# Kernel tuning notes

Measured on AMD Instinct MI355X. Metric: run time of the kernel, lower is better.

## Reference

```python
import math
import jax, jax.numpy as jnp
import numpy as np

B, S, D, H = 2, 2048, 1024, 16
DH = D // H
EPS = 1e-5


def setup_inputs() -> dict:
    key = jax.random.key(0)
    ks = jax.random.split(key, 8)
    def lin(k, din, dout):
        return jax.random.normal(k, (din, dout), dtype=jnp.float32) / math.sqrt(din)
    return {
        "x": jax.random.normal(ks[0], (B, S, D), dtype=jnp.float32),
        "attention_mask": jnp.ones((B, S), dtype=jnp.int32),
        "Wq": lin(ks[1], D, D),
        "Wk": lin(ks[2], D, D),
        "Wv": lin(ks[3], D, D),
        "Wo": lin(ks[4], D, D),
        "W1": lin(ks[5], D, 4 * D),
        "W2": lin(ks[6], 2 * D, D),
        "gamma1": jnp.ones((D,), jnp.float32),
        "beta1": jnp.zeros((D,), jnp.float32),
        "gamma2": jnp.ones((D,), jnp.float32),
        "beta2": jnp.zeros((D,), jnp.float32),
    }


def layernorm(x, gamma, beta):
    mu = jnp.mean(x, axis=-1, keepdims=True)
    xc = x - mu
    var = jnp.mean(xc * xc, axis=-1, keepdims=True)
    return gamma * (xc / jnp.sqrt(var + EPS)) + beta


def softmax_last(x):
    x = x - jnp.max(x, axis=-1, keepdims=True)
    e = jnp.exp(x)
    return e / jnp.sum(e, axis=-1, keepdims=True)


def mhsa(x, attention_mask, Wq, Wk, Wv, Wo, causal=True):
    b, s, d = x.shape
    q = (x @ Wq).reshape(b, s, H, DH).transpose(0, 2, 1, 3)  # [b,h,s,dh]
    k = (x @ Wk).reshape(b, s, H, DH).transpose(0, 2, 1, 3)
    v = (x @ Wv).reshape(b, s, H, DH).transpose(0, 2, 1, 3)
    score = jnp.einsum("bhqd,bhkd->bhqk", q, k) / math.sqrt(DH)
    if causal:
        cmask = jnp.tril(jnp.ones((s, s), dtype=bool))
        score = jnp.where(cmask[None, None], score, -jnp.inf)
    key_mask = attention_mask.astype(bool)[:, None, None, :]  # [b,1,1,s]
    score = jnp.where(key_mask, score, -jnp.inf)
    attn = softmax_last(score)
    out = jnp.einsum("bhqk,bhkd->bhqd", attn, v)
    out = out.transpose(0, 2, 1, 3).reshape(b, s, d)
    return out @ Wo


def reference(x, attention_mask, Wq, Wk, Wv, Wo, W1, W2, gamma1, beta1, gamma2, beta2):
    x1 = x + mhsa(layernorm(x, gamma1, beta1), attention_mask, Wq, Wk, Wv, Wo, causal=True)
    h = layernorm(x1, gamma2, beta2) @ W1          # [b,s,4d]
    left, right = h[:, :, : 2 * D], h[:, :, 2 * D :]
    glu = left * jax.nn.sigmoid(right)             # [b,s,2d]
    return x1 + glu @ W2
```

## Files before the change

kernel.cpp:

```cpp
#include <hip/hip_runtime.h>
#include <hip/hip_bf16.h>
#include <math.h>

#define BB 2
#define SS 2048
#define DD 1024
#define HH 16
#define DH 64
#define NTOK (BB * SS)
#define LN_EPS 1e-5f
#define BIGNEG -1e30f

typedef __attribute__((ext_vector_type(8))) short bf16x8;
typedef __attribute__((ext_vector_type(4))) float f32x4;

static __device__ __forceinline__ unsigned short f2bu(float f) {
    __hip_bfloat16 h = __float2bfloat16(f);
    return *(unsigned short*)&h;
}

static __device__ __forceinline__ void async16(const void* g, void* l) {
    __builtin_amdgcn_global_load_lds((const __attribute__((address_space(1))) void*)g,
                                     (__attribute__((address_space(3))) void*)l, 16, 0, 0);
}


__global__ __launch_bounds__(256) void prep_kernel(const float* __restrict__ Wq,
                                                   const float* __restrict__ Wk,
                                                   const float* __restrict__ Wv,
                                                   const float* __restrict__ Wo,
                                                   const float* __restrict__ W1,
                                                   const float* __restrict__ W2,
                                                   __hip_bfloat16* __restrict__ wqkvt,
                                                   __hip_bfloat16* __restrict__ wot,
                                                   __hip_bfloat16* __restrict__ w1t,
                                                   __hip_bfloat16* __restrict__ w2t,
                                                   const float* __restrict__ x,
                                                   const float* __restrict__ gamma,
                                                   const float* __restrict__ beta,
                                                   __hip_bfloat16* __restrict__ lnb) {
    __shared__ float t[32][33];
    __shared__ float red[256];
    const int bid = blockIdx.x;
    const int tid = threadIdx.x;

    if (bid >= 10240) {
        const int row = bid - 10240;
        const float* xp = x + (size_t)row * DD;
        float vals[4];
        float s = 0.f;
#pragma unroll
        for (int i = 0; i < 4; ++i) {
            float v = xp[tid + i * 256];
            vals[i] = v;
            s += v;
        }
        red[tid] = s;
        __syncthreads();
        for (int st = 128; st > 0; st >>= 1) {
            if (tid < st) red[tid] += red[tid + st];
            __syncthreads();
        }
        const float mu = red[0] * (1.0f / DD);
        __syncthreads();
        float sq = 0.f;
#pragma unroll
        for (int i = 0; i < 4; ++i) {
            float d = vals[i] - mu;
            sq += d * d;
        }
        red[tid] = sq;
        __syncthreads();
        for (int st = 128; st > 0; st >>= 1) {
            if (tid < st) red[tid] += red[tid + st];
            __syncthreads();
        }
        const float rinv = rsqrtf(red[0] * (1.0f / DD) + LN_EPS);
        __hip_bfloat16* op = lnb + (size_t)row * DD;
#pragma unroll
        for (int i = 0; i < 4; ++i) {
            int j = tid + i * 256;
            op[j] = __float2bfloat16(gamma[j] * ((vals[i] - mu) * rinv) + beta[j]);
        }
        return;
    }

    const float* W;
    __hip_bfloat16* Wt;
    int K, N, tile;
    if (bid < 4096) {
        const int m = bid >> 10;
        tile = bid & 1023;
        W = (m == 0) ? Wq : (m == 1) ? Wk : (m == 2) ? Wv : Wo;
        Wt = (m < 3) ? (wqkvt + (size_t)m * 1024 * 1024) : wot;
        K = 1024; N = 1024;
    } else if (bid < 8192) {
        tile = bid - 4096; W = W1; Wt = w1t; K = 1024; N = 4096;
    } else {
        tile = bid - 8192; W = W2; Wt = w2t; K = 2048; N = 1024;
    }
    const int nt = N >> 5;
    const int n0 = (tile % nt) * 32, k0 = (tile / nt) * 32;
    const int tx = tid & 31, ty = tid >> 5;
#pragma unroll
    for (int i = 0; i < 4; ++i)
        t[ty + 8 * i][tx] = W[(size_t)(k0 + ty + 8 * i) * N + n0 + tx];
    __syncthreads();
#pragma unroll
    for (int i = 0; i < 4; ++i)
        Wt[(size_t)(n0 + ty + 8 * i) * K + k0 + tx] = __float2bfloat16(t[tx][ty + 8 * i]);
}

__global__ __launch_bounds__(256) void ln_kernel(const float* __restrict__ x,
                                                 const float* __restrict__ gamma,
                                                 const float* __restrict__ beta,
                                                 __hip_bfloat16* __restrict__ out) {
    const int row = blockIdx.x;
    const int tid = threadIdx.x;
    __shared__ float red[256];

    const float* xp = x + (size_t)row * DD;
    float vals[4];
    float s = 0.f;
#pragma unroll
    for (int i = 0; i < 4; ++i) {
        float v = xp[tid + i * 256];
        vals[i] = v;
        s += v;
    }
    red[tid] = s;
    __syncthreads();
    for (int st = 128; st > 0; st >>= 1) {
        if (tid < st) red[tid] += red[tid + st];
        __syncthreads();
    }
    const float mu = red[0] * (1.0f / DD);
    __syncthreads();
    float sq = 0.f;
#pragma unroll
    for (int i = 0; i < 4; ++i) {
        float d = vals[i] - mu;
        sq += d * d;
    }
    red[tid] = sq;
    __syncthreads();
    for (int st = 128; st > 0; st >>= 1) {
        if (tid < st) red[tid] += red[tid + st];
        __syncthreads();
    }
    const float rinv = rsqrtf(red[0] * (1.0f / DD) + LN_EPS);

    __hip_bfloat16* op = out + (size_t)row * DD;
#pragma unroll
    for (int i = 0; i < 4; ++i) {
        int j = tid + i * 256;
        op[j] = __float2bfloat16(gamma[j] * ((vals[i] - mu) * rinv) + beta[j]);
    }
}

__global__ __launch_bounds__(256) void vtrans(const __hip_bfloat16* __restrict__ qkvb_,
                                              __hip_bfloat16* __restrict__ VT_) {
    const unsigned short* src = (const unsigned short*)qkvb_;
    unsigned short* dst = (unsigned short*)VT_;
    __shared__ unsigned short t[64][65];
    const int c0 = (blockIdx.x & 15) << 6;
    const int t0 = (blockIdx.x >> 4) << 6;
    const int tx = threadIdx.x & 63, ty = threadIdx.x >> 6;
#pragma unroll
    for (int i = 0; i < 16; ++i)
        t[ty + 4 * i][tx] = src[(size_t)(t0 + ty + 4 * i) * 3072 + 2048 + c0 + tx];
    __syncthreads();
#pragma unroll
    for (int i = 0; i < 16; ++i)
        dst[(size_t)(c0 + ty + 4 * i) * 4096 + t0 + tx] = t[tx][ty + 4 * i];
}

template <int RES, int EPI>
__global__ __launch_bounds__(256) void mfma_gemm(const __hip_bfloat16* __restrict__ A,
                                                 const __hip_bfloat16* __restrict__ Bt,
                                                 const void* __restrict__ res,
                                                 void* __restrict__ out,
                                                 int M, int N, int K) {
    __shared__ short As[128 * 64];
    __shared__ short Bs[128 * 64];
    const int tid = threadIdx.x;
    const int lane = tid & 63;
    const int wave = tid >> 6;
    const int row0 = blockIdx.y * 128;
    const int col0 = blockIdx.x * 128;
    const int wr = (wave >> 1) * 64;
    const int wc = (wave & 1) * 64;
    const int l15 = lane & 15;
    const int quad = lane >> 4;
    const int s7 = l15 & 7;

    f32x4 acc[4][4] = {};

    for (int k0 = 0; k0 < K; k0 += 64) {
#pragma unroll
        for (int r = 0; r < 4; ++r) {
            const int ec = r * 256 + tid;
            const int ar = ec >> 3, d = ec & 7;
            const int ao = (d ^ (ar & 7)) << 3;
            async16(&A[(size_t)(row0 + ar) * K + k0 + ao], &As[ec << 3]);
            async16(&Bt[(size_t)(col0 + ar) * K + k0 + ao], &Bs[ec << 3]);
        }
        __syncthreads();
#pragma unroll
        for (int kk = 0; kk < 2; ++kk) {
            const int co = (((kk << 2) | quad) ^ s7) << 3;
            bf16x8 af[4], bfr[4];
#pragma unroll
            for (int i = 0; i < 4; ++i)
                af[i] = *(const bf16x8*)&As[(wr + i * 16 + l15) * 64 + co];
#pragma unroll
            for (int j = 0; j < 4; ++j)
                bfr[j] = *(const bf16x8*)&Bs[(wc + j * 16 + l15) * 64 + co];
#pragma unroll
            for (int i = 0; i < 4; ++i)
#pragma unroll
                for (int j = 0; j < 4; ++j)
                    acc[i][j] = __builtin_amdgcn_mfma_f32_16x16x32_bf16(af[i], bfr[j], acc[i][j], 0, 0, 0);
        }
        __syncthreads();
    }

    const int r4 = quad * 4;
#pragma unroll
    for (int i = 0; i < 4; ++i) {
#pragma unroll
        for (int j = 0; j < 4; ++j) {
            const int orow0 = row0 + wr + i * 16 + r4;
            const int ocol = col0 + wc + j * 16 + l15;
#pragma unroll
            for (int rg = 0; rg < 4; ++rg) {
                const size_t oi = (size_t)(orow0 + rg) * N + ocol;
                float v = acc[i][j][rg];
                if constexpr (RES == 1) v += ((const float*)res)[oi];
                if constexpr (EPI == 0) ((float*)out)[oi] = v;
                if constexpr (EPI == 1) ((__hip_bfloat16*)out)[oi] = __float2bfloat16(v);
            }
        }
    }
}

template <int RES, int EPI>
__global__ __launch_bounds__(256) void mfma_gemm_n64(const __hip_bfloat16* __restrict__ A,
                                                     const __hip_bfloat16* __restrict__ Bt,
                                                     const void* __restrict__ res,
                                                     void* __restrict__ out,
                                                     int N, int K, int colTiles) {
    __shared__ short As[128 * 64];
    __shared__ short Bs[64 * 64];
    const int tid = threadIdx.x;
    const int lane = tid & 63;
    const int wave = tid >> 6;
    const int cpx = gridDim.x >> 3;
    const int wg = (blockIdx.x & 7) * cpx + (blockIdx.x >> 3);
    const int row0 = (wg / colTiles) * 128;
    const int col0 = (wg % colTiles) * 64;
    const int wr = wave * 32;
    const int l15 = lane & 15;
    const int quad = lane >> 4;
    const int s7 = l15 & 7;

    f32x4 acc[2][4] = {};

    for (int k0 = 0; k0 < K; k0 += 64) {
#pragma unroll
        for (int r = 0; r < 4; ++r) {
            const int ec = r * 256 + tid;
            const int ar = ec >> 3, d = ec & 7;
            const int ao = (d ^ (ar & 7)) << 3;
            async16(&A[(size_t)(row0 + ar) * K + k0 + ao], &As[ec << 3]);
        }
#pragma unroll
        for (int r = 0; r < 2; ++r) {
            const int ec = r * 256 + tid;
            const int ar = ec >> 3, d = ec & 7;
            const int ao = (d ^ (ar & 7)) << 3;
            async16(&Bt[(size_t)(col0 + ar) * K + k0 + ao], &Bs[ec << 3]);
        }
        __syncthreads();
#pragma unroll
        for (int kk = 0; kk < 2; ++kk) {
            const int co = (((kk << 2) | quad) ^ s7) << 3;
            bf16x8 af[2], bfr[4];
#pragma unroll
            for (int i = 0; i < 2; ++i)
                af[i] = *(const bf16x8*)&As[(wr + i * 16 + l15) * 64 + co];
#pragma unroll
            for (int j = 0; j < 4; ++j)
                bfr[j] = *(const bf16x8*)&Bs[(j * 16 + l15) * 64 + co];
#pragma unroll
            for (int i = 0; i < 2; ++i)
#pragma unroll
                for (int j = 0; j < 4; ++j)
                    acc[i][j] = __builtin_amdgcn_mfma_f32_16x16x32_bf16(af[i], bfr[j], acc[i][j], 0, 0, 0);
        }
        __syncthreads();
    }

    const int r4 = quad * 4;
#pragma unroll
    for (int i = 0; i < 2; ++i) {
#pragma unroll
        for (int j = 0; j < 4; ++j) {
            const int orow0 = row0 + wr + i * 16 + r4;
            const int ocol = col0 + j * 16 + l15;
#pragma unroll
            for (int rg = 0; rg < 4; ++rg) {
                const size_t oi = (size_t)(orow0 + rg) * N + ocol;
                float v = acc[i][j][rg];
                if constexpr (RES == 1) v += ((const float*)res)[oi];
                if constexpr (EPI == 0) ((float*)out)[oi] = v;
                if constexpr (EPI == 1) ((__hip_bfloat16*)out)[oi] = __float2bfloat16(v);
            }
        }
    }
}

__global__ __launch_bounds__(256) void mfma_gemm_glu64(const __hip_bfloat16* __restrict__ A,
                                                       const __hip_bfloat16* __restrict__ Bt,
                                                       __hip_bfloat16* __restrict__ out) {
    __shared__ short As[128 * 64];
    __shared__ short Bl[64 * 64];
    __shared__ short Br[64 * 64];
    const int tid = threadIdx.x;
    const int lane = tid & 63;
    const int wave = tid >> 6;
    const int cpx = gridDim.x >> 3;
    const int wg = (blockIdx.x & 7) * cpx + (blockIdx.x >> 3);
    const int row0 = (wg >> 5) * 128;
    const int col0 = (wg & 31) * 64;
    const int wr = wave * 32;
    const int l15 = lane & 15;
    const int quad = lane >> 4;
    const int s7 = l15 & 7;

    f32x4 accl[2][4] = {};
    f32x4 accr[2][4] = {};

    for (int k0 = 0; k0 < 1024; k0 += 64) {
#pragma unroll
        for (int r = 0; r < 4; ++r) {
            const int ec = r * 256 + tid;
            const int ar = ec >> 3, d = ec & 7;
            const int ao = (d ^ (ar & 7)) << 3;
            async16(&A[(size_t)(row0 + ar) * 1024 + k0 + ao], &As[ec << 3]);
        }
#pragma unroll
        for (int r = 0; r < 2; ++r) {
            const int ec = r * 256 + tid;
            const int ar = ec >> 3, d = ec & 7;
            const int ao = (d ^ (ar & 7)) << 3;
            async16(&Bt[(size_t)(col0 + ar) * 1024 + k0 + ao], &Bl[ec << 3]);
            async16(&Bt[(size_t)(2048 + col0 + ar) * 1024 + k0 + ao], &Br[ec << 3]);
        }
        __syncthreads();
#pragma unroll
        for (int kk = 0; kk < 2; ++kk) {
            const int co = (((kk << 2) | quad) ^ s7) << 3;
            bf16x8 af[2], bl[4], br[4];
#pragma unroll
            for (int i = 0; i < 2; ++i)
                af[i] = *(const bf16x8*)&As[(wr + i * 16 + l15) * 64 + co];
#pragma unroll
            for (int j = 0; j < 4; ++j) {
                bl[j] = *(const bf16x8*)&Bl[(j * 16 + l15) * 64 + co];
                br[j] = *(const bf16x8*)&Br[(j * 16 + l15) * 64 + co];
            }
#pragma unroll
            for (int i = 0; i < 2; ++i)
#pragma unroll
                for (int j = 0; j < 4; ++j) {
                    accl[i][j] = __builtin_amdgcn_mfma_f32_16x16x32_bf16(af[i], bl[j], accl[i][j], 0, 0, 0);
                    accr[i][j] = __builtin_amdgcn_mfma_f32_16x16x32_bf16(af[i], br[j], accr[i][j], 0, 0, 0);
                }
        }
        __syncthreads();
    }

    const int r4 = quad * 4;
#pragma unroll
    for (int i = 0; i < 2; ++i) {
#pragma unroll
        for (int j = 0; j < 4; ++j) {
#pragma unroll
            for (int rg = 0; rg < 4; ++rg) {
                const int orow = row0 + wr + i * 16 + r4 + rg;
                const int ocol = col0 + j * 16 + l15;
                const float l = accl[i][j][rg];
                const float r = accr[i][j][rg];
                out[(size_t)orow * 2048 + ocol] =
                    __float2bfloat16(l * (1.f / (1.f + __expf(-r))));
            }
        }
    }
}

#define KADV (64 * 3072)
#define RESCALE_THR 8.f
__global__ __launch_bounds__(256, 4) void flash_mfma(const __hip_bfloat16* __restrict__ qkv_,
                                                     const __hip_bfloat16* __restrict__ VT_,
                                                     const int* __restrict__ mask,
                                                     __hip_bfloat16* __restrict__ attnb) {
    const unsigned short* qkv = (const unsigned short*)qkv_;
    const unsigned short* VT = (const unsigned short*)VT_;
    __shared__ __align__(16) short Ks[2][64 * 64];
    __shared__ __align__(16) short Vt[2][64 * 64];
    __shared__ __align__(16) short Ps[4][16 * 64];

    const int tid = threadIdx.x;
    const int lane = tid & 63;
    const int wave = tid >> 6;
    const int l15 = lane & 15;
    const int quad = lane >> 4;
    const int s7 = l15 & 7;

    const int xcd = blockIdx.x & 7;
    const int slot = blockIdx.x >> 3;
    const int bh = xcd + ((slot & 3) << 3);
    const int v = slot >> 2;
    const int vr = v & 7, vs = v >> 3;
    const int qt = (vs == 0) ? 31 - vr : (vs == 1) ? vr : (vs == 2) ? 23 - vr : 8 + vr;
    const int h = bh & 15;
    const int b = bh >> 4;
    const int q0 = qt * 64 + wave * 16;

    const int e0 = tid, e1 = 256 + tid;
    const int r0 = e0 >> 3, d0 = e0 & 7, r1 = e1 >> 3, d1 = e1 & 7;
    const unsigned short* kp0 = qkv + (size_t)(b * SS + r0) * 3072 + 1024 + h * 64 + ((d0 ^ (r0 & 7)) << 3);
    const unsigned short* kp1 = qkv + (size_t)(b * SS + r1) * 3072 + 1024 + h * 64 + ((d1 ^ (r1 & 7)) << 3);
    const unsigned short* vp0 = VT + (size_t)(h * 64 + r0) * 4096 + b * SS + ((d0 ^ (r0 & 7)) << 3);
    const unsigned short* vp1 = VT + (size_t)(h * 64 + r1) * 4096 + b * SS + ((d1 ^ (r1 & 7)) << 3);
    short* const kd0a = &Ks[0][e0 << 3]; short* const kd0b = &Ks[1][e0 << 3];
    short* const kd1a = &Ks[0][e1 << 3]; short* const kd1b = &Ks[1][e1 << 3];
    short* const vd0a = &Vt[0][e0 << 3]; short* const vd0b = &Vt[1][e0 << 3];
    short* const vd1a = &Vt[0][e1 << 3]; short* const vd1b = &Vt[1][e1 << 3];

    const int* const mrow = mask + b * SS;

    bf16x8 aq[2];
#pragma unroll
    for (int ks = 0; ks < 2; ++ks)
        aq[ks] = *(const bf16x8*)(qkv + (size_t)(b * SS + q0 + l15) * 3072 +
                                  h * 64 + ks * 32 + quad * 8);

    f32x4 O[4];
    float m_r[4], l_r[4];
#pragma unroll
    for (int i = 0; i < 4; ++i) {
        O[i] = (f32x4){0.f, 0.f, 0.f, 0.f};
        m_r[i] = BIGNEG;
        l_r[i] = 0.f;
    }

    const int nch = qt + 1;

    async16(kp0, kd0a); async16(kp1, kd1a);
    async16(vp0, vd0a); async16(vp1, vd1a);
    kp0 += KADV; kp1 += KADV; vp0 += 64; vp1 += 64;

    for (int c = 0; c < nch; ++c) {
        const int cur = c & 1;
        __syncthreads();

        if (c + 1 < nch) {
            async16(kp0, cur ? kd0a : kd0b);
            async16(kp1, cur ? kd1a : kd1b);
            async16(vp0, cur ? vd0a : vd0b);
            async16(vp1, cur ? vd1a : vd1b);
            kp0 += KADV; kp1 += KADV; vp0 += 64; vp1 += 64;
        }

        const int kb = c << 6;
        const int dq = q0 - kb;
        if (dq + 15 < 0) continue;

        int ktmax = ((dq + 15) >> 4) + 1;
        if (ktmax > 4) ktmax = 4;
        int ktfull = (dq - 15) >= 0 ? ((dq - 15) >> 4) + 1 : 0;
        if (ktfull > 4) ktfull = 4;
        const short* Kc = &Ks[cur][0];
        const short* Vc = &Vt[cur][0];

        int mv[4];
#pragma unroll
        for (int kt = 0; kt < 4; ++kt) {
            if (kt >= ktmax) break;
            mv[kt] = mrow[kb + kt * 16 + l15];
        }

        f32x4 S[4];
        __builtin_amdgcn_s_setprio(1);
#pragma unroll
        for (int kt = 0; kt < 4; ++kt) {
            if (kt >= ktmax) break;
            const bf16x8 bk0 = *(const bf16x8*)&Kc[(kt * 16 + l15) * 64 + ((quad ^ s7) << 3)];
            const bf16x8 bk1 = *(const bf16x8*)&Kc[(kt * 16 + l15) * 64 + (((4 | quad) ^ s7) << 3)];
            f32x4 z = {0.f, 0.f, 0.f, 0.f};
            z = __builtin_amdgcn_mfma_f32_16x16x32_bf16(aq[0], bk0, z, 0, 0, 0);
            S[kt] = __builtin_amdgcn_mfma_f32_16x16x32_bf16(aq[1], bk1, z, 0, 0, 0);
        }
        __builtin_amdgcn_s_setprio(0);
#pragma unroll
        for (int kt = 0; kt < 4; ++kt) {
            if (kt >= ktmax) break;
            const float bv = mv[kt] ? 0.f : BIGNEG;
#pragma unroll
            for (int rg = 0; rg < 4; ++rg) {
                float s = fmaf(S[kt][rg], 0.125f, bv);
                if (kt >= ktfull) {
                    const int key = kb + kt * 16 + l15;
                    const int qrow = q0 + quad * 4 + rg;
                    s = (key <= qrow) ? s : BIGNEG;
                }
                S[kt][rg] = s;
            }
        }
        float tmax[4];
#pragma unroll
        for (int rg = 0; rg < 4; ++rg) {
            float v2 = BIGNEG;
#pragma unroll
            for (int kt = 0; kt < 4; ++kt)
                if (kt < ktmax) v2 = fmaxf(v2, S[kt][rg]);
            v2 = fmaxf(v2, __shfl_xor(v2, 1));
            v2 = fmaxf(v2, __shfl_xor(v2, 2));
            v2 = fmaxf(v2, __shfl_xor(v2, 4));
            v2 = fmaxf(v2, __shfl_xor(v2, 8));
            tmax[rg] = v2;
        }
        bool grow = false;
#pragma unroll
        for (int rg = 0; rg < 4; ++rg)
            grow = grow || (tmax[rg] > m_r[rg] + RESCALE_THR);
        if (__any(grow)) {
            float alpha[4];
#pragma unroll
            for (int rg = 0; rg < 4; ++rg) {
                const float mn = fmaxf(m_r[rg], tmax[rg]);
                alpha[rg] = __expf(m_r[rg] - mn);
                m_r[rg] = mn;
                l_r[rg] *= alpha[rg];
            }
#pragma unroll
            for (int nt = 0; nt < 4; ++nt)
#pragma unroll
                for (int rg = 0; rg < 4; ++rg)
                    O[nt][rg] *= alpha[rg];
        }
#pragma unroll
        for (int kt = 0; kt < 4; ++kt) {
            if (kt >= ktmax) break;
#pragma unroll
            for (int rg = 0; rg < 4; ++rg)
                S[kt][rg] = __expf(S[kt][rg] - m_r[rg]);
        }
#pragma unroll
        for (int rg = 0; rg < 4; ++rg) {
            float v2 = 0.f;
#pragma unroll
            for (int kt = 0; kt < 4; ++kt)
                if (kt < ktmax) v2 += S[kt][rg];
            v2 += __shfl_xor(v2, 1);
            v2 += __shfl_xor(v2, 2);
            v2 += __shfl_xor(v2, 4);
            v2 += __shfl_xor(v2, 8);
            l_r[rg] += v2;
        }

        short* Pw = &Ps[wave][0];
        asm volatile("s_waitcnt lgkmcnt(0)" ::: "memory");
#pragma unroll
        for (int kt = 0; kt < 4; ++kt) {
            if (kt >= ktmax) break;
#pragma unroll
            for (int rg = 0; rg < 4; ++rg) {
                const int qr = quad * 4 + rg;
                const int ch = (kt * 2) | (l15 >> 3);
                Pw[(qr << 6) + (((ch ^ (qr & 7)) << 3) | s7)] = (short)f2bu(S[kt][rg]);
            }
        }
        const int kkmax = (ktmax + 1) >> 1;
        if (ktmax & 1) {
#pragma unroll
            for (int rg = 0; rg < 4; ++rg) {
                const int qr = quad * 4 + rg;
                const int ch = (ktmax * 2) | (l15 >> 3);
                Pw[(qr << 6) + (((ch ^ (qr & 7)) << 3) | s7)] = 0;
            }
        }
        asm volatile("s_waitcnt lgkmcnt(0)" ::: "memory");
        __builtin_amdgcn_s_setprio(1);
#pragma unroll
        for (int kk = 0; kk < 2; ++kk) {
            if (kk >= kkmax) break;
            const bf16x8 ap = *(const bf16x8*)&Pw[(l15 << 6) + ((((kk << 2) | quad) ^ s7) << 3)];
#pragma unroll
            for (int nt = 0; nt < 4; ++nt) {
                const bf16x8 bv = *(const bf16x8*)&Vc[(nt * 16 + l15) * 64 +
                                                     ((((kk << 2) | quad) ^ s7) << 3)];
                O[nt] = __builtin_amdgcn_mfma_f32_16x16x32_bf16(ap, bv, O[nt], 0, 0, 0);
            }
        }
        __builtin_amdgcn_s_setprio(0);
    }

#pragma unroll
    for (int rg = 0; rg < 4; ++rg) {
        const int q = q0 + quad * 4 + rg;
        const float inv = 1.f / l_r[rg];
        unsigned short* op = (unsigned short*)attnb + (size_t)(b * SS + q) * 1024 + h * 64;
#pragma unroll
        for (int nt = 0; nt < 4; ++nt)
            op[nt * 16 + l15] = f2bu(O[nt][rg] * inv);
    }
}

extern "C" void kernel_launch(void* const* d_in, const int* in_sizes, int n_in,
                              void* d_out, int out_size, void* d_ws, size_t ws_size,
                              hipStream_t stream) {
    const float* x  = (const float*)d_in[0];
    const int* mask = (const int*)d_in[1];
    const float* Wq = (const float*)d_in[2];
    const float* Wk = (const float*)d_in[3];
    const float* Wv = (const float*)d_in[4];
    const float* Wo = (const float*)d_in[5];
    const float* W1 = (const float*)d_in[6];
    const float* W2 = (const float*)d_in[7];
    const float* g1 = (const float*)d_in[8];
    const float* b1 = (const float*)d_in[9];
    const float* g2 = (const float*)d_in[10];
    const float* b2 = (const float*)d_in[11];

    const size_t MB = 1024 * 1024;
    uint8_t* ws = (uint8_t*)d_ws;
    __hip_bfloat16* wqkvt = (__hip_bfloat16*)(ws);
    __hip_bfloat16* wot   = (__hip_bfloat16*)(ws + 6 * MB);
    __hip_bfloat16* w1t   = (__hip_bfloat16*)(ws + 8 * MB);
    __hip_bfloat16* w2t   = (__hip_bfloat16*)(ws + 16 * MB);
    __hip_bfloat16* lnb   = (__hip_bfloat16*)(ws + 20 * MB);
    __hip_bfloat16* qkvb  = (__hip_bfloat16*)(ws + 28 * MB);
    float*          x1    = (float*)(ws + 28 * MB);
    __hip_bfloat16* attnb = (__hip_bfloat16*)(ws + 52 * MB);
    __hip_bfloat16* VT    = (__hip_bfloat16*)(ws + 60 * MB);
    __hip_bfloat16* glub  = (__hip_bfloat16*)(ws + 68 * MB);

    prep_kernel<<<10240 + NTOK, 256, 0, stream>>>(Wq, Wk, Wv, Wo, W1, W2,
                                                  wqkvt, wot, w1t, w2t,
                                                  x, g1, b1, lnb);

    mfma_gemm<0, 1><<<dim3(24, 32), 256, 0, stream>>>(lnb, wqkvt, nullptr, qkvb, NTOK, 3072, 1024);

    vtrans<<<1024, 256, 0, stream>>>(qkvb, VT);

    flash_mfma<<<1024, 256, 0, stream>>>(qkvb, VT, mask, attnb);

    mfma_gemm_n64<1, 0><<<512, 256, 0, stream>>>(attnb, wot, x, x1, 1024, 1024, 16);

    ln_kernel<<<NTOK, 256, 0, stream>>>(x1, g2, b2, lnb);

    mfma_gemm_glu64<<<1024, 256, 0, stream>>>(lnb, w1t, glub);

    mfma_gemm_n64<1, 0><<<512, 256, 0, stream>>>(glub, w2t, x1, (float*)d_out,
                                                 1024, 2048, 16);
}
```

Before: 222.5 us.

## Transpose attention MFMA operands so each lane owns one query row

Swaps the A/B operands of the QK^T and PV MFMAs so the accumulator layout puts the query row on the lane index and keys or head-dims in the register group. Each lane then keeps a single running max and sum instead of four, which cuts the row reductions from four cross-lane shuffle chains to two shuffles each. It also lets P be written to LDS as packed 32-bit words and the output be written as 64-bit packed bf16 stores. The mask is now loaded as int4 vectors. Correctness depends on the new index mapping for the causal mask, the swizzled P layout and the output matching the swapped operands.

```diff
diff --git a/kernel.cpp b/kernel.cpp
--- a/kernel.cpp
+++ b/kernel.cpp
@@ -448,13 +448,9 @@
                                   h * 64 + ks * 32 + quad * 8);
 
     f32x4 O[4];
-    float m_r[4], l_r[4];
-#pragma unroll
-    for (int i = 0; i < 4; ++i) {
-        O[i] = (f32x4){0.f, 0.f, 0.f, 0.f};
-        m_r[i] = BIGNEG;
-        l_r[i] = 0.f;
-    }
+#pragma unroll
+    for (int i = 0; i < 4; ++i) O[i] = (f32x4){0.f, 0.f, 0.f, 0.f};
+    float m_r = BIGNEG, l_r = 0.f;
 
     const int nch = qt + 1;
 
@@ -485,11 +481,11 @@
         const short* Kc = &Ks[cur][0];
         const short* Vc = &Vt[cur][0];
 
-        int mv[4];
+        int4 mv[4];
 #pragma unroll
         for (int kt = 0; kt < 4; ++kt) {
             if (kt >= ktmax) break;
-            mv[kt] = mrow[kb + kt * 16 + l15];
+            mv[kt] = *(const int4*)&mrow[kb + kt * 16 + quad * 4];
         }
 
         f32x4 S[4];
@@ -500,122 +496,108 @@
             const bf16x8 bk0 = *(const bf16x8*)&Kc[(kt * 16 + l15) * 64 + ((quad ^ s7) << 3)];
             const bf16x8 bk1 = *(const bf16x8*)&Kc[(kt * 16 + l15) * 64 + (((4 | quad) ^ s7) << 3)];
             f32x4 z = {0.f, 0.f, 0.f, 0.f};
-            z = __builtin_amdgcn_mfma_f32_16x16x32_bf16(aq[0], bk0, z, 0, 0, 0);
-            S[kt] = __builtin_amdgcn_mfma_f32_16x16x32_bf16(aq[1], bk1, z, 0, 0, 0);
+            z = __builtin_amdgcn_mfma_f32_16x16x32_bf16(bk0, aq[0], z, 0, 0, 0);
+            S[kt] = __builtin_amdgcn_mfma_f32_16x16x32_bf16(bk1, aq[1], z, 0, 0, 0);
         }
         __builtin_amdgcn_s_setprio(0);
+
+        const int qrow = q0 + l15;
 #pragma unroll
         for (int kt = 0; kt < 4; ++kt) {
             if (kt >= ktmax) break;
-            const float bv = mv[kt] ? 0.f : BIGNEG;
+            const int* mm = (const int*)&mv[kt];
 #pragma unroll
             for (int rg = 0; rg < 4; ++rg) {
-                float s = fmaf(S[kt][rg], 0.125f, bv);
+                float s = fmaf(S[kt][rg], 0.125f, mm[rg] ? 0.f : BIGNEG);
                 if (kt >= ktfull) {
-                    const int key = kb + kt * 16 + l15;
-                    const int qrow = q0 + quad * 4 + rg;
+                    const int key = kb + kt * 16 + quad * 4 + rg;
                     s = (key <= qrow) ? s : BIGNEG;
                 }
                 S[kt][rg] = s;
             }
         }
-        float tmax[4];
-#pragma unroll
-        for (int rg = 0; rg < 4; ++rg) {
-            float v2 = BIGNEG;
-#pragma unroll
-            for (int kt = 0; kt < 4; ++kt)
-                if (kt < ktmax) v2 = fmaxf(v2, S[kt][rg]);
-            v2 = fmaxf(v2, __shfl_xor(v2, 1));
-            v2 = fmaxf(v2, __shfl_xor(v2, 2));
-            v2 = fmaxf(v2, __shfl_xor(v2, 4));
-            v2 = fmaxf(v2, __shfl_xor(v2, 8));
-            tmax[rg] = v2;
-        }
-        bool grow = false;
-#pragma unroll
-        for (int rg = 0; rg < 4; ++rg)
-            grow = grow || (tmax[rg] > m_r[rg] + RESCALE_THR);
-        if (__any(grow)) {
-            float alpha[4];
-#pragma unroll
-            for (int rg = 0; rg < 4; ++rg) {
-                const float mn = fmaxf(m_r[rg], tmax[rg]);
-                alpha[rg] = __expf(m_r[rg] - mn);
-                m_r[rg] = mn;
-                l_r[rg] *= alpha[rg];
-            }
-#pragma unroll
-            for (int nt = 0; nt < 4; ++nt)
-#pragma unroll
-                for (int rg = 0; rg < 4; ++rg)
-                    O[nt][rg] *= alpha[rg];
-        }
+
+        float tmax = BIGNEG;
 #pragma unroll
         for (int kt = 0; kt < 4; ++kt) {
             if (kt >= ktmax) break;
+            tmax = fmaxf(tmax, fmaxf(fmaxf(S[kt][0], S[kt][1]),
+                                     fmaxf(S[kt][2], S[kt][3])));
+        }
+        tmax = fmaxf(tmax, __shfl_xor(tmax, 16));
+        tmax = fmaxf(tmax, __shfl_xor(tmax, 32));
+
+        if (__any(tmax > m_r + RESCALE_THR)) {
+            const float mn = fmaxf(m_r, tmax);
+            const float alpha = __expf(m_r - mn);
+            m_r = mn;
+            l_r *= alpha;
+#pragma unroll
+            for (int nt = 0; nt < 4; ++nt)
+#pragma unroll
+                for (int rg = 0; rg < 4; ++rg)
+                    O[nt][rg] *= alpha;
+        }
+
+        float rsum = 0.f;
+#pragma unroll
+        for (int kt = 0; kt < 4; ++kt) {
+            if (kt >= ktmax) break;
 #pragma unroll
             for (int rg = 0; rg < 4; ++rg)
-                S[kt][rg] = __expf(S[kt][rg] - m_r[rg]);
-        }
-#pragma unroll
-        for (int rg = 0; rg < 4; ++rg) {
-            float v2 = 0.f;
-#pragma unroll
-            for (int kt = 0; kt < 4; ++kt)
-                if (kt < ktmax) v2 += S[kt][rg];
-            v2 += __shfl_xor(v2, 1);
-            v2 += __shfl_xor(v2, 2);
-            v2 += __shfl_xor(v2, 4);
-            v2 += __shfl_xor(v2, 8);
-            l_r[rg] += v2;
-        }
+                S[kt][rg] = __expf(S[kt][rg] - m_r);
+            rsum += (S[kt][0] + S[kt][1]) + (S[kt][2] + S[kt][3]);
+        }
+        rsum += __shfl_xor(rsum, 16);
+        rsum += __shfl_xor(rsum, 32);
+        l_r += rsum;
 
         short* Pw = &Ps[wave][0];
         asm volatile("s_waitcnt lgkmcnt(0)" ::: "memory");
 #pragma unroll
         for (int kt = 0; kt < 4; ++kt) {
             if (kt >= ktmax) break;
-#pragma unroll
-            for (int rg = 0; rg < 4; ++rg) {
-                const int qr = quad * 4 + rg;
-                const int ch = (kt * 2) | (l15 >> 3);
-                Pw[(qr << 6) + (((ch ^ (qr & 7)) << 3) | s7)] = (short)f2bu(S[kt][rg]);
-            }
+            const int ch = (kt << 1) | (quad >> 1);
+            const int base = (l15 << 6) + (((ch ^ s7) << 3) | ((quad & 1) << 2));
+            const unsigned p0 = ((unsigned)f2bu(S[kt][1]) << 16) | f2bu(S[kt][0]);
+            const unsigned p1 = ((unsigned)f2bu(S[kt][3]) << 16) | f2bu(S[kt][2]);
+            *(unsigned*)&Pw[base] = p0;
+            *(unsigned*)&Pw[base + 2] = p1;
         }
         const int kkmax = (ktmax + 1) >> 1;
         if (ktmax & 1) {
-#pragma unroll
-            for (int rg = 0; rg < 4; ++rg) {
-                const int qr = quad * 4 + rg;
-                const int ch = (ktmax * 2) | (l15 >> 3);
-                Pw[(qr << 6) + (((ch ^ (qr & 7)) << 3) | s7)] = 0;
-            }
+            const int ch = (ktmax << 1) | (quad >> 1);
+            const int base = (l15 << 6) + (((ch ^ s7) << 3) | ((quad & 1) << 2));
+            *(unsigned*)&Pw[base] = 0;
+            *(unsigned*)&Pw[base + 2] = 0;
         }
         asm volatile("s_waitcnt lgkmcnt(0)" ::: "memory");
         __builtin_amdgcn_s_setprio(1);
 #pragma unroll
         for (int kk = 0; kk < 2; ++kk) {
             if (kk >= kkmax) break;
-            const bf16x8 ap = *(const bf16x8*)&Pw[(l15 << 6) + ((((kk << 2) | quad) ^ s7) << 3)];
+            const bf16x8 bp = *(const bf16x8*)&Pw[(l15 << 6) + ((((kk << 2) | quad) ^ s7) << 3)];
 #pragma unroll
             for (int nt = 0; nt < 4; ++nt) {
-                const bf16x8 bv = *(const bf16x8*)&Vc[(nt * 16 + l15) * 64 +
+                const bf16x8 av = *(const bf16x8*)&Vc[(nt * 16 + l15) * 64 +
                                                      ((((kk << 2) | quad) ^ s7) << 3)];
-                O[nt] = __builtin_amdgcn_mfma_f32_16x16x32_bf16(ap, bv, O[nt], 0, 0, 0);
+                O[nt] = __builtin_amdgcn_mfma_f32_16x16x32_bf16(av, bp, O[nt], 0, 0, 0);
             }
         }
         __builtin_amdgcn_s_setprio(0);
     }
 
-#pragma unroll
-    for (int rg = 0; rg < 4; ++rg) {
-        const int q = q0 + quad * 4 + rg;
-        const float inv = 1.f / l_r[rg];
-        unsigned short* op = (unsigned short*)attnb + (size_t)(b * SS + q) * 1024 + h * 64;
-#pragma unroll
-        for (int nt = 0; nt < 4; ++nt)
-            op[nt * 16 + l15] = f2bu(O[nt][rg] * inv);
+    const float inv = 1.f / l_r;
+    unsigned short* op = (unsigned short*)attnb +
+                         (size_t)(b * SS + q0 + l15) * 1024 + h * 64 + quad * 4;
+#pragma unroll
+    for (int nt = 0; nt < 4; ++nt) {
+        const float o0 = O[nt][0] * inv, o1 = O[nt][1] * inv;
+        const float o2 = O[nt][2] * inv, o3 = O[nt][3] * inv;
+        const unsigned long long pk =
+            (unsigned long long)(((unsigned)f2bu(o3) << 16) | f2bu(o2)) << 32 |
+            (((unsigned)f2bu(o1) << 16) | f2bu(o0));
+        *(unsigned long long*)(op + nt * 16) = pk;
     }
 }
 
```

Measured after the change: 209.9 us. 5.7% less time.
